# Performance work log

Measured on AMD Instinct MI355X. Metric: run time of the kernel, lower is better.

Reference implementation:

```python
import jax, jax.numpy as jnp
import numpy as np

NUM_SENSORS = 4
D_MODEL = 64
N_HEAD = 8
HEAD_DIM = 8
EPS_LN = 1e-5
EPS_BN = 1e-5
A_BASE = np.array([[1, 1, 0, 0], [1, 1, 1, 1], [0, 1, 1, 1], [0, 1, 1, 1]], dtype=np.float32)


def _pos_encoding(S, D):
    pos = jnp.arange(S, dtype=jnp.float32)[:, None]
    div = jnp.exp(jnp.arange(0, D, 2, dtype=jnp.float32) * (-jnp.log(jnp.float32(10000.0)) / D))
    pe = jnp.zeros((S, D), jnp.float32)
    pe = pe.at[:, 0::2].set(jnp.sin(pos * div))
    pe = pe.at[:, 1::2].set(jnp.cos(pos * div))
    return pe


def _ln(x, g, b):
    m = x.mean(-1, keepdims=True)
    v = ((x - m) ** 2).mean(-1, keepdims=True)
    return (x - m) * jax.lax.rsqrt(v + EPS_LN) * g + b


def _conv1d(x, w, b, stride, pad):
    y = jax.lax.conv_general_dilated(x, w, (stride,), [(pad, pad)], dimension_numbers=('NCH', 'OIH', 'NCH'))
    return y + b[None, :, None]


def _maxpool2(x):  # [B,C,L] -> [B,C,L//2]
    B, C, L = x.shape
    return x[:, :, : (L // 2) * 2].reshape(B, C, L // 2, 2).max(-1)


def _bn_eval(x, g, b):  # eval-mode BN with fresh running stats (mean=0, var=1)
    scale = g * jax.lax.rsqrt(jnp.float32(1.0 + EPS_BN))
    return x * scale[None, :, None] + b[None, :, None]


def _mha(x, wqkv, bqkv, wo, bo):
    B, S, D = x.shape
    qkv = x @ wqkv.T + bqkv  # [B,S,3D]
    q, k, v = jnp.split(qkv, 3, -1)
    heads = lambda t: t.reshape(B, S, N_HEAD, HEAD_DIM).transpose(0, 2, 1, 3)
    q, k, v = heads(q), heads(k), heads(v)
    scores = jnp.einsum('bhqd,bhkd->bhqk', q, k) / jnp.float32(np.sqrt(HEAD_DIM))
    attn = jax.nn.softmax(scores, -1)
    out = jnp.einsum('bhqk,bhkd->bhqd', attn, v).transpose(0, 2, 1, 3).reshape(B, S, D)
    return out @ wo.T + bo


def _encoder_layer(x, wqkv, bqkv, wo, bo, ln1g, ln1b, w1, b1, w2, b2, ln2g, ln2b):
    # torch post-norm (norm_first=False), gelu, dropout off (eval)
    x = _ln(x + _mha(x, wqkv, bqkv, wo, bo), ln1g, ln1b)
    ff = jax.nn.gelu(x @ w1.T + b1, approximate=False) @ w2.T + b2
    return _ln(x + ff, ln2g, ln2b)


def _branch(x, bp):
    h = x.transpose(0, 2, 1)  # [B,1,L]
    h = _maxpool2(jax.nn.relu(_bn_eval(_conv1d(h, bp['c1w'], bp['c1b'], 2, 2), bp['g1'], bp['be1'])))
    h = _maxpool2(jax.nn.relu(_bn_eval(_conv1d(h, bp['c2w'], bp['c2b'], 1, 1), bp['g2'], bp['be2'])))
    h = h.transpose(0, 2, 1)  # [B,S,64], S = L/8
    h = h + _pos_encoding(h.shape[1], D_MODEL)
    for l in range(2):
        h = _encoder_layer(h, bp['wqkv'][l], bp['bqkv'][l], bp['wo'][l], bp['bo'][l],
                           bp['ln1g'][l], bp['ln1b'][l], bp['fw1'][l], bp['fb1'][l],
                           bp['fw2'][l], bp['fb2'][l], bp['ln2g'][l], bp['ln2b'][l])
    return h.mean(1)  # [B,64]


def _gcn(x, A, W, b):
    # PyG GCNConv with edge weights over the dense per-sample 4x4 graph
    deg = A.sum(1)  # deg[b,j] = sum_i A[b,i,j]  (scatter over dst)
    dinv = jnp.where(deg > 0, 1.0 / jnp.sqrt(jnp.where(deg > 0, deg, 1.0)), 0.0)
    norm = dinv[:, :, None] * A * dinv[:, None, :]  # [B,N,N]
    return jnp.einsum('bij,bif->bjf', norm, x @ W) + b


def _forward(sensor_data, conv1_w, conv1_b, bn1_g, bn1_b, conv2_w, conv2_b, bn2_g, bn2_b,
             attn_wqkv, attn_bqkv, attn_wo, attn_bo, ln1_g, ln1_b, ff_w1, ff_b1, ff_w2, ff_b2,
             ln2_g, ln2_b, ws_w, ws_b, b_s, lambda_init, mc_w1, mc_b1, mc_w2, mc_b2,
             gcn1_w, gcn1_b, gcn2_w, gcn2_b, cls_w1, cls_b1, cls_w2, cls_b2, epoch):
    feats = []
    for i in range(NUM_SENSORS):
        bp = dict(c1w=conv1_w[i], c1b=conv1_b[i], g1=bn1_g[i], be1=bn1_b[i],
                  c2w=conv2_w[i], c2b=conv2_b[i], g2=bn2_g[i], be2=bn2_b[i],
                  wqkv=attn_wqkv[i], bqkv=attn_bqkv[i], wo=attn_wo[i], bo=attn_bo[i],
                  ln1g=ln1_g[i], ln1b=ln1_b[i], fw1=ff_w1[i], fb1=ff_b1[i],
                  fw2=ff_w2[i], fb2=ff_b2[i], ln2g=ln2_g[i], ln2b=ln2_b[i])
        feats.append(_branch(sensor_data[i], bp))
    nf = jnp.stack(feats, 1)  # [B,4,64]
    # dynamic adjacency: sigmoid(W_s([f_i;f_j]) + b_s) for all pairs, vectorized
    wa, wb = ws_w[:D_MODEL], ws_w[D_MODEL:]
    fa = nf @ wa  # [B,4]
    fb = nf @ wb
    s = jax.nn.sigmoid(fa[:, :, None] + fb[:, None, :] + ws_b + b_s)  # [B,4,4]
    deg = s.sum(-1)  # row degree deg[b,i]
    a = s / (deg[:, None, :] + 1e-8)  # == bmm(s, eye * 1/(deg+eps))
    S_hat = jax.nn.relu(a * jnp.asarray(A_BASE))
    lam = jax.nn.sigmoid(jax.nn.relu(nf.mean(1) @ mc_w1.T + mc_b1) @ mc_w2 + mc_b2) * lambda_init  # [B]
    lam = lam[:, None, None]
    A = lam * jnp.eye(NUM_SENSORS, dtype=jnp.float32) + (1.0 - lam) * S_hat  # A_prev = I (first call)
    # tau_0 is undefined in the source; tau treated as 0 => threshold is a no-op (A >= 0)
    h = jax.nn.relu(_gcn(nf, A, gcn1_w, gcn1_b))  # [B,4,128]
    g = _gcn(h, A, gcn2_w, gcn2_b).mean(1)  # [B,256]
    return jax.nn.relu(g @ cls_w1 + cls_b1) @ cls_w2 + cls_b2  # [B,5]


def setup_inputs() -> dict:
    key = jax.random.key(0)
    ks = iter(jax.random.split(key, 64))
    rn = lambda shape, s: jax.random.normal(next(ks), shape, jnp.float32) * s
    S4, B, L = 4, 64, 2048
    return {
        'sensor_data': jax.random.normal(next(ks), (S4, B, L, 1), jnp.float32),
        'conv1_w': rn((S4, 32, 1, 5), 0.3), 'conv1_b': rn((S4, 32), 0.02),
        'bn1_g': jnp.ones((S4, 32), jnp.float32), 'bn1_b': jnp.zeros((S4, 32), jnp.float32),
        'conv2_w': rn((S4, 64, 32, 3), 0.1), 'conv2_b': rn((S4, 64), 0.02),
        'bn2_g': jnp.ones((S4, 64), jnp.float32), 'bn2_b': jnp.zeros((S4, 64), jnp.float32),
        'attn_wqkv': rn((S4, 2, 192, 64), 0.08), 'attn_bqkv': rn((S4, 2, 192), 0.02),
        'attn_wo': rn((S4, 2, 64, 64), 0.08), 'attn_bo': rn((S4, 2, 64), 0.02),
        'ln1_g': jnp.ones((S4, 2, 64), jnp.float32), 'ln1_b': jnp.zeros((S4, 2, 64), jnp.float32),
        'ff_w1': rn((S4, 2, 256, 64), 0.08), 'ff_b1': rn((S4, 2, 256), 0.02),
        'ff_w2': rn((S4, 2, 64, 256), 0.06), 'ff_b2': rn((S4, 2, 64), 0.02),
        'ln2_g': jnp.ones((S4, 2, 64), jnp.float32), 'ln2_b': jnp.zeros((S4, 2, 64), jnp.float32),
        'ws_w': rn((128,), 0.08), 'ws_b': rn((), 0.02), 'b_s': jnp.zeros((), jnp.float32),
        'lambda_init': jnp.asarray(0.5, jnp.float32),
        'mc_w1': rn((32, 64), 0.1), 'mc_b1': rn((32,), 0.02),
        'mc_w2': rn((32,), 0.15), 'mc_b2': rn((), 0.02),
        'gcn1_w': rn((64, 128), 0.1), 'gcn1_b': rn((128,), 0.02),
        'gcn2_w': rn((128, 256), 0.08), 'gcn2_b': rn((256,), 0.02),
        'cls_w1': rn((256, 128), 0.08), 'cls_b1': rn((128,), 0.02),
        'cls_w2': rn((128, 5), 0.1), 'cls_b2': rn((5,), 0.02),
        'epoch': 1,
    }


def reference(sensor_data, conv1_w, conv1_b, bn1_g, bn1_b, conv2_w, conv2_b, bn2_g, bn2_b,
              attn_wqkv, attn_bqkv, attn_wo, attn_bo, ln1_g, ln1_b, ff_w1, ff_b1, ff_w2, ff_b2,
              ln2_g, ln2_b, ws_w, ws_b, b_s, lambda_init, mc_w1, mc_b1, mc_w2, mc_b2,
              gcn1_w, gcn1_b, gcn2_w, gcn2_b, cls_w1, cls_b1, cls_w2, cls_b2, epoch):
    return _forward(sensor_data, conv1_w, conv1_b, bn1_g, bn1_b, conv2_w, conv2_b, bn2_g, bn2_b,
                    attn_wqkv, attn_bqkv, attn_wo, attn_bo, ln1_g, ln1_b, ff_w1, ff_b1, ff_w2, ff_b2,
                    ln2_g, ln2_b, ws_w, ws_b, b_s, lambda_init, mc_w1, mc_b1, mc_w2, mc_b2,
                    gcn1_w, gcn1_b, gcn2_w, gcn2_b, cls_w1, cls_b1, cls_w2, cls_b2, epoch)
```

## Files before the change

kernel.cpp:

```cpp
#include <hip/hip_runtime.h>
#include <hip/hip_fp16.h>

#define NSENS 4
#define NB    64
#define LIN   2048
#define C1N   32
#define LP1   512
#define C2N   64
#define SEQ   256
#define DM    64

typedef _Float16 f16x4 __attribute__((ext_vector_type(4)));
typedef _Float16 f16x8 __attribute__((ext_vector_type(8)));
typedef float    f32x4 __attribute__((ext_vector_type(4)));

#define MFMA16(A,B,C) __builtin_amdgcn_mfma_f32_16x16x16f16((A),(B),(C),0,0,0)
#define MFMA32(A,B,C) __builtin_amdgcn_mfma_f32_16x16x32_f16((A),(B),(C),0,0,0)

__device__ __forceinline__ float fast_exp2(float x) {
#if __has_builtin(__builtin_amdgcn_exp2f)
  return __builtin_amdgcn_exp2f(x);
#else
  return exp2f(x);
#endif
}

__device__ __forceinline__ char* swp(char* base, int row, int stride, int byteoff) {
  return base + row*stride + ((byteoff & ~15) ^ ((row & 7) << 4)) + (byteoff & 15);
}
__device__ __forceinline__ float sr_h(char* base, int row, int stride, int col) {
  return (float)*(const _Float16*)swp(base, row, stride, col*2);
}
__device__ __forceinline__ void pack8(char* p, float4 a, float4 b) {
  __half2 h0 = __floats2half2_rn(a.x,a.y), h1 = __floats2half2_rn(a.z,a.w);
  __half2 h2 = __floats2half2_rn(b.x,b.y), h3 = __floats2half2_rn(b.z,b.w);
  uint4 u; u.x=*(unsigned*)&h0; u.y=*(unsigned*)&h1; u.z=*(unsigned*)&h2; u.w=*(unsigned*)&h3;
  *(uint4*)p = u;
}
__device__ __forceinline__ uint2 pack4u(float a, float b, float cc, float d) {
  __half2 h0 = __floats2half2_rn(a, b), h1 = __floats2half2_rn(cc, d);
  uint2 u; u.x = *(unsigned*)&h0; u.y = *(unsigned*)&h1; return u;
}

__global__ __launch_bounds__(256) void wprep_kernel(
    const float* __restrict__ wqkv, const float* __restrict__ wo,
    const float* __restrict__ fw1,  const float* __restrict__ fw2,
    unsigned short* __restrict__ w16)
{
  const int wi = blockIdx.x;
  unsigned short* dst = w16 + (size_t)wi*49152;
  const float* s0 = wqkv + (size_t)wi*12288;
  const float* s1 = wo   + (size_t)wi*4096;
  const float* s2 = fw1  + (size_t)wi*16384;
  const float* s3 = fw2  + (size_t)wi*16384;
  for (int i = threadIdx.x; i < 12288; i += 256) { __half h = __float2half_rn(s0[i]); dst[i]       = *(unsigned short*)&h; }
  for (int i = threadIdx.x; i < 4096;  i += 256) { __half h = __float2half_rn(s1[i]); dst[12288+i] = *(unsigned short*)&h; }
  for (int i = threadIdx.x; i < 16384; i += 256) { __half h = __float2half_rn(s2[i]); dst[16384+i] = *(unsigned short*)&h; }
  for (int i = threadIdx.x; i < 16384; i += 256) { __half h = __float2half_rn(s3[i]); dst[32768+i] = *(unsigned short*)&h; }
}

__global__ __launch_bounds__(1024, 1) void tx_kernel(
  const float* __restrict__ sens,
  const float* __restrict__ c1w, const float* __restrict__ c1b,
  const float* __restrict__ bn1g, const float* __restrict__ bn1b,
  const float* __restrict__ c2w, const float* __restrict__ c2b,
  const float* __restrict__ bn2g, const float* __restrict__ bn2b,
  float* __restrict__ nf,
  const unsigned short* __restrict__ w16,
  const float* __restrict__ bqkv, const float* __restrict__ bo,
  const float* __restrict__ ln1g, const float* __restrict__ ln1b,
  const float* __restrict__ fb1,  const float* __restrict__ fb2,
  const float* __restrict__ ln2g, const float* __restrict__ ln2b)
{
  __shared__ char smem[132096];
  char* xs = smem;
  char* Qb = smem + 32768;
  char* Kb = smem + 65536;
  char* Vt = smem + 98304;
  float* red = (float*)(smem + 131072);

  const int bid = blockIdx.x;
  const int s = bid >> 6, b = bid & 63;
  const int t = threadIdx.x;
  const int l = t & 63, w = t >> 6;
  const int g = l >> 4, c = l & 15;
  const int m0 = w * 16;
  const float qs = 0.35355339059327373f * 1.4426950408889634f;

  {
    __half (*h1p)[516] = (__half(*)[516])(smem + 32768);
    float* w2s = (float*)(smem + 65792);

    for (int i = t; i < C1N*3*C2N; i += 1024) {
      int co = i & 63; int rem = i >> 6; int k = rem % 3; int ci = rem / 3;
      w2s[(ci*3 + k)*64 + co] = c2w[((s*C2N + co)*C1N + ci)*3 + k];
    }
    const float* xg = sens + (size_t)(s*NB + b)*LIN;
    const float bnr = rsqrtf(1.0f + 1e-5f);
    {
      const int cc1 = t & 31;
      const int l0 = t >> 5;
      const float w0 = c1w[(s*C1N + cc1)*5 + 0];
      const float w1 = c1w[(s*C1N + cc1)*5 + 1];
      const float w2 = c1w[(s*C1N + cc1)*5 + 2];
      const float w3 = c1w[(s*C1N + cc1)*5 + 3];
      const float w4 = c1w[(s*C1N + cc1)*5 + 4];
      const float cb = c1b[s*C1N + cc1];
      const float sc = bn1g[s*C1N + cc1]*bnr;
      const float bt = bn1b[s*C1N + cc1];
      for (int ll = l0; ll < LP1; ll += 32) {
        const int base = 4*ll;
        float xm2 = (base-2 >= 0) ? xg[base-2] : 0.f;
        float xm1 = (base-1 >= 0) ? xg[base-1] : 0.f;
        float x0v = xg[base+0];
        float x1v = xg[base+1];
        float x2v = xg[base+2];
        float x3v = xg[base+3];
        float x4v = (base+4 < LIN) ? xg[base+4] : 0.f;
        float y0 = w0*xm2 + w1*xm1 + w2*x0v + w3*x1v + w4*x2v;
        float y1 = w0*x0v + w1*x1v + w2*x2v + w3*x3v + w4*x4v;
        y0 = (y0 + cb)*sc + bt;
        y1 = (y1 + cb)*sc + bt;
        h1p[cc1][ll+1] = __float2half(fmaxf(fmaxf(y0, y1), 0.f));
        if (ll == 0)      h1p[cc1][0]      = __float2half(0.f);
        if (ll == LP1-1)  h1p[cc1][LP1+1]  = __float2half(0.f);
      }
    }
    __syncthreads();
    {
      const int r = t & 255, q = t >> 8;
      float acc0[16], acc1[16];
      #pragma unroll
      for (int i = 0; i < 16; ++i) { acc0[i] = 0.f; acc1[i] = 0.f; }
      for (int ci = 0; ci < C1N; ++ci) {
        const __half2 a01 = *(const __half2*)&h1p[ci][2*r];
        const __half2 a23 = *(const __half2*)&h1p[ci][2*r+2];
        const float2 f01 = __half22float2(a01);
        const float2 f23 = __half22float2(a23);
        const float hx[4] = { f01.x, f01.y, f23.x, f23.y };
        #pragma unroll
        for (int k = 0; k < 3; ++k) {
          const float* wrow = w2s + (ci*3+k)*64 + q*16;
          const float4 wv0 = *(const float4*)(wrow + 0);
          const float4 wv1 = *(const float4*)(wrow + 4);
          const float4 wv2 = *(const float4*)(wrow + 8);
          const float4 wv3 = *(const float4*)(wrow + 12);
          const float wr[16] = {wv0.x,wv0.y,wv0.z,wv0.w, wv1.x,wv1.y,wv1.z,wv1.w,
                                wv2.x,wv2.y,wv2.z,wv2.w, wv3.x,wv3.y,wv3.z,wv3.w};
          const float xa = hx[k], xb = hx[k+1];
          #pragma unroll
          for (int i = 0; i < 16; ++i) {
            acc0[i] = fmaf(wr[i], xa, acc0[i]);
            acc1[i] = fmaf(wr[i], xb, acc1[i]);
          }
        }
      }
      float vv[16];
      #pragma unroll
      for (int i = 0; i < 16; ++i) {
        const int d = q*16 + i;
        const float cb2 = c2b[s*C2N + d];
        const float sc2 = bn2g[s*C2N + d]*bnr;
        const float bt2 = bn2b[s*C2N + d];
        float v0 = (acc0[i] + cb2)*sc2 + bt2;
        float v1 = (acc1[i] + cb2)*sc2 + bt2;
        float v = fmaxf(fmaxf(v0, v1), 0.f);
        const float ang = (float)r * __expf(-0.14391156463f*(float)(d & ~1));
        const float pe = (d & 1) ? cosf(ang) : sinf(ang);
        vv[i] = v + pe;
      }
      pack8(swp(xs, r, 128, q*32),
            make_float4(vv[0],vv[1],vv[2],vv[3]), make_float4(vv[4],vv[5],vv[6],vv[7]));
      pack8(swp(xs, r, 128, q*32 + 16),
            make_float4(vv[8],vv[9],vv[10],vv[11]), make_float4(vv[12],vv[13],vv[14],vv[15]));
    }
  }
  __syncthreads();

  for (int layer = 0; layer < 2; ++layer) {
    const int wi = s*2 + layer;
    const unsigned short* wq = w16 + (size_t)wi*49152;
    const unsigned short* wo = wq + 12288;
    const unsigned short* w1 = wq + 16384;
    const unsigned short* w2 = wq + 32768;
    const float* Bq  = bqkv + wi*192;
    const float* Bo  = bo   + wi*64;
    const float* G1  = ln1g + wi*64; const float* B1 = ln1b + wi*64;
    const float* Bf1 = fb1  + wi*256; const float* Bf2 = fb2 + wi*64;
    const float* G2  = ln2g + wi*64; const float* B2 = ln2b + wi*64;

    {
      f16x8 xf0 = *(const f16x8*)swp(xs, m0+c, 128, 0  + g*16);
      f16x8 xf1 = *(const f16x8*)swp(xs, m0+c, 128, 64 + g*16);
      #pragma unroll
      for (int nt = 0; nt < 4; ++nt) {
        const int row = 64 + nt*16 + c;
        f16x8 w0f = *(const f16x8*)(wq + row*64 + 8*g);
        f16x8 w1f = *(const f16x8*)(wq + row*64 + 32 + 8*g);
        f32x4 d = {0.f,0.f,0.f,0.f};
        d = MFMA32(w0f, xf0, d); d = MFMA32(w1f, xf1, d);
        float4 b4 = *(const float4*)(Bq + 64 + nt*16 + 4*g);
        *(uint2*)swp(Kb, m0+c, 128, nt*32 + 8*g) =
            pack4u(d[0]+b4.x, d[1]+b4.y, d[2]+b4.z, d[3]+b4.w);
      }
      #pragma unroll
      for (int nt = 0; nt < 4; ++nt) {
        const int row = nt*16 + c;
        f16x8 w0f = *(const f16x8*)(wq + row*64 + 8*g);
        f16x8 w1f = *(const f16x8*)(wq + row*64 + 32 + 8*g);
        f32x4 d = {0.f,0.f,0.f,0.f};
        d = MFMA32(w0f, xf0, d); d = MFMA32(w1f, xf1, d);
        float4 b4 = *(const float4*)(Bq + nt*16 + 4*g);
        *(uint2*)swp(Qb, m0+c, 128, nt*32 + 8*g) =
            pack4u((d[0]+b4.x)*qs, (d[1]+b4.y)*qs, (d[2]+b4.z)*qs, (d[3]+b4.w)*qs);
      }
      #pragma unroll
      for (int nt = 0; nt < 4; ++nt) {
        const int row = 128 + nt*16 + c;
        f16x8 w0f = *(const f16x8*)(wq + row*64 + 8*g);
        f16x8 w1f = *(const f16x8*)(wq + row*64 + 32 + 8*g);
        f32x4 d = {0.f,0.f,0.f,0.f};
        d = MFMA32(xf0, w0f, d); d = MFMA32(xf1, w1f, d);
        const float bias = Bq[128 + nt*16 + c];
        *(uint2*)swp(Vt, nt*16+c, 512, 32*w + 8*g) =
            pack4u(d[0]+bias, d[1]+bias, d[2]+bias, d[3]+bias);
      }
    }
    __syncthreads();

    #pragma unroll 2
    for (int task = 0; task < 8; ++task) {
      const int h = task;
      f16x4 qb = {0,0,0,0};
      if (g < 2) qb = *(const f16x4*)swp(Qb, m0+c, 128, 16*h + 8*g);
      f32x4 o = {0.f,0.f,0.f,0.f};
      #pragma unroll
      for (int jt = 0; jt < 16; ++jt) {
        f16x4 ka = *(const f16x4*)swp(Kb, jt*16+c, 128, (16*h + 8*g) & 127);
        f32x4 st = {0.f,0.f,0.f,0.f};
        st = MFMA16(ka, qb, st);
        uint2 pu = pack4u(fast_exp2(st[0]), fast_exp2(st[1]),
                          fast_exp2(st[2]), fast_exp2(st[3]));
        f16x4 pb = *(f16x4*)&pu;
        f16x4 va;
        if (c < 8) va = *(const f16x4*)swp(Vt, 8*h+c, 512, jt*32 + (g>>1)*16 + (g&1)*8);
        else { va[0]=(_Float16)1.f; va[1]=(_Float16)1.f; va[2]=(_Float16)1.f; va[3]=(_Float16)1.f; }
        o = MFMA16(va, pb, o);
      }
      const float den = __shfl(o[0], 32 + c, 64);
      const float rinv = 1.0f / den;
      if (g < 2) {
        *(uint2*)swp(Qb, m0+c, 128, 16*h + 8*g) =
            pack4u(o[0]*rinv, o[1]*rinv, o[2]*rinv, o[3]*rinv);
      }
    }
    __syncthreads();

    {
      f16x8 ab0 = *(const f16x8*)swp(Qb, m0+c, 128, 0  + g*16);
      f16x8 ab1 = *(const f16x8*)swp(Qb, m0+c, 128, 64 + g*16);
      float vals[4][4];
      #pragma unroll
      for (int nt = 0; nt < 4; ++nt) {
        f16x8 w0f = *(const f16x8*)(wo + (nt*16+c)*64 + 8*g);
        f16x8 w1f = *(const f16x8*)(wo + (nt*16+c)*64 + 32 + 8*g);
        f32x4 d = {0.f,0.f,0.f,0.f};
        d = MFMA32(w0f, ab0, d); d = MFMA32(w1f, ab1, d);
        float4 b4 = *(const float4*)(Bo + nt*16 + 4*g);
        uint2 rr = *(uint2*)swp(xs, m0+c, 128, nt*32 + 8*g);
        float2 r0 = __half22float2(*(__half2*)&rr.x);
        float2 r1 = __half22float2(*(__half2*)&rr.y);
        vals[nt][0] = d[0] + b4.x + r0.x;
        vals[nt][1] = d[1] + b4.y + r0.y;
        vals[nt][2] = d[2] + b4.z + r1.x;
        vals[nt][3] = d[3] + b4.w + r1.y;
      }
      float p1 = 0.f, p2 = 0.f;
      #pragma unroll
      for (int nt = 0; nt < 4; ++nt)
        #pragma unroll
        for (int i = 0; i < 4; ++i) { p1 += vals[nt][i]; p2 = fmaf(vals[nt][i], vals[nt][i], p2); }
      p1 += __shfl_xor(p1, 16, 64); p1 += __shfl_xor(p1, 32, 64);
      p2 += __shfl_xor(p2, 16, 64); p2 += __shfl_xor(p2, 32, 64);
      const float mean = p1*(1.0f/64.0f);
      const float rstd = rsqrtf(p2*(1.0f/64.0f) - mean*mean + 1e-5f);
      #pragma unroll
      for (int nt = 0; nt < 4; ++nt) {
        float4 g4 = *(const float4*)(G1 + nt*16 + 4*g);
        float4 b4 = *(const float4*)(B1 + nt*16 + 4*g);
        *(uint2*)swp(xs, m0+c, 128, nt*32 + 8*g) =
            pack4u((vals[nt][0]-mean)*rstd*g4.x + b4.x,
                   (vals[nt][1]-mean)*rstd*g4.y + b4.y,
                   (vals[nt][2]-mean)*rstd*g4.z + b4.z,
                   (vals[nt][3]-mean)*rstd*g4.w + b4.w);
      }
    }

    {
      f16x8 xb0 = *(const f16x8*)swp(xs, m0+c, 128, 0  + g*16);
      f16x8 xb1 = *(const f16x8*)swp(xs, m0+c, 128, 64 + g*16);
      f32x4 o2[4];
      #pragma unroll
      for (int nt2 = 0; nt2 < 4; ++nt2) { o2[nt2][0]=0.f; o2[nt2][1]=0.f; o2[nt2][2]=0.f; o2[nt2][3]=0.f; }
      #pragma unroll
      for (int ht = 0; ht < 16; ++ht) {
        f16x8 w0f = *(const f16x8*)(w1 + (ht*16+c)*64 + 8*g);
        f16x8 w1f = *(const f16x8*)(w1 + (ht*16+c)*64 + 32 + 8*g);
        f32x4 d = {0.f,0.f,0.f,0.f};
        d = MFMA32(w0f, xb0, d); d = MFMA32(w1f, xb1, d);
        float4 bf4 = *(const float4*)(Bf1 + ht*16 + 4*g);
        float h0 = d[0] + bf4.x, h1 = d[1] + bf4.y, h2 = d[2] + bf4.z, h3 = d[3] + bf4.w;
        h0 = 0.5f*h0*(1.0f + erff(h0*0.70710678118654752f));
        h1 = 0.5f*h1*(1.0f + erff(h1*0.70710678118654752f));
        h2 = 0.5f*h2*(1.0f + erff(h2*0.70710678118654752f));
        h3 = 0.5f*h3*(1.0f + erff(h3*0.70710678118654752f));
        uint2 pu = pack4u(h0, h1, h2, h3);
        f16x4 pf = *(f16x4*)&pu;
        #pragma unroll
        for (int nt2 = 0; nt2 < 4; ++nt2) {
          f16x4 a2 = *(const f16x4*)(w2 + (nt2*16+c)*256 + ht*16 + 4*g);
          o2[nt2] = MFMA16(a2, pf, o2[nt2]);
        }
      }
      float vals[4][4];
      #pragma unroll
      for (int nt2 = 0; nt2 < 4; ++nt2) {
        float4 b4 = *(const float4*)(Bf2 + nt2*16 + 4*g);
        uint2 rr = *(uint2*)swp(xs, m0+c, 128, nt2*32 + 8*g);
        float2 r0 = __half22float2(*(__half2*)&rr.x);
        float2 r1 = __half22float2(*(__half2*)&rr.y);
        vals[nt2][0] = o2[nt2][0] + b4.x + r0.x;
        vals[nt2][1] = o2[nt2][1] + b4.y + r0.y;
        vals[nt2][2] = o2[nt2][2] + b4.z + r1.x;
        vals[nt2][3] = o2[nt2][3] + b4.w + r1.y;
      }
      float p1 = 0.f, p2 = 0.f;
      #pragma unroll
      for (int nt2 = 0; nt2 < 4; ++nt2)
        #pragma unroll
        for (int i = 0; i < 4; ++i) { p1 += vals[nt2][i]; p2 = fmaf(vals[nt2][i], vals[nt2][i], p2); }
      p1 += __shfl_xor(p1, 16, 64); p1 += __shfl_xor(p1, 32, 64);
      p2 += __shfl_xor(p2, 16, 64); p2 += __shfl_xor(p2, 32, 64);
      const float mean = p1*(1.0f/64.0f);
      const float rstd = rsqrtf(p2*(1.0f/64.0f) - mean*mean + 1e-5f);
      #pragma unroll
      for (int nt2 = 0; nt2 < 4; ++nt2) {
        float4 g4 = *(const float4*)(G2 + nt2*16 + 4*g);
        float4 b4 = *(const float4*)(B2 + nt2*16 + 4*g);
        *(uint2*)swp(xs, m0+c, 128, nt2*32 + 8*g) =
            pack4u((vals[nt2][0]-mean)*rstd*g4.x + b4.x,
                   (vals[nt2][1]-mean)*rstd*g4.y + b4.y,
                   (vals[nt2][2]-mean)*rstd*g4.z + b4.z,
                   (vals[nt2][3]-mean)*rstd*g4.w + b4.w);
      }
    }
  }

  __syncthreads();
  if (t < 256) {
    const int d = t & 63, qu = t >> 6;
    float sm = 0.f;
    for (int rr = qu*64; rr < qu*64 + 64; ++rr) sm += sr_h(xs, rr, 128, d);
    red[qu*64 + d] = sm;
  }
  __syncthreads();
  if (t < 64) {
    float sm = red[t] + red[64+t] + red[128+t] + red[192+t];
    nf[((size_t)b*4 + s)*64 + t] = sm * (1.0f/256.0f);
  }
}

__global__ __launch_bounds__(128) void head_kernel(
  const float* __restrict__ nf,
  const float* __restrict__ ws_w, const float* __restrict__ ws_b,
  const float* __restrict__ b_s,  const float* __restrict__ lambda_init,
  const float* __restrict__ mc_w1, const float* __restrict__ mc_b1,
  const float* __restrict__ mc_w2, const float* __restrict__ mc_b2,
  const float* __restrict__ g1w, const float* __restrict__ g1b,
  const float* __restrict__ g2w, const float* __restrict__ g2b,
  const float* __restrict__ cw1, const float* __restrict__ cb1,
  const float* __restrict__ cw2, const float* __restrict__ cb2,
  float* __restrict__ out)
{
  const int b = blockIdx.x, t = threadIdx.x;
  __shared__ float nfb[256];
  __shared__ float meannf[64];
  __shared__ float fafb[8];
  __shared__ float z1[32];
  __shared__ float normM[16];
  __shared__ float rs[4];
  __shared__ float xw[512];
  __shared__ float hmat[512];
  __shared__ float hw[1024];
  __shared__ float gv[256];
  __shared__ float r1[128];

  for (int i = t; i < 256; i += 128) nfb[i] = nf[b*256 + i];
  __syncthreads();
  if (t < 8) {
    const int i = t & 3;
    const float* w = ws_w + (t >> 2)*64;
    float acc = 0.f;
    for (int c = 0; c < 64; ++c) acc = fmaf(nfb[i*64+c], w[c], acc);
    fafb[t] = acc;
  }
  if (t >= 64 && t < 128) {
    const int d = t - 64;
    meannf[d] = 0.25f*(nfb[d] + nfb[64+d] + nfb[128+d] + nfb[192+d]);
  }
  __syncthreads();
  if (t < 32) {
    float acc = mc_b1[t];
    const float* w = mc_w1 + t*64;
    for (int c = 0; c < 64; ++c) acc = fmaf(meannf[c], w[c], acc);
    z1[t] = fmaxf(acc, 0.f);
  }
  __syncthreads();
  if (t == 0) {
    float li = mc_b2[0];
    for (int k = 0; k < 32; ++k) li = fmaf(z1[k], mc_w2[k], li);
    const float lam = (1.0f/(1.0f + __expf(-li))) * lambda_init[0];
    const float AB[4][4] = {{1,1,0,0},{1,1,1,1},{0,1,1,1},{0,1,1,1}};
    const float add = ws_b[0] + b_s[0];
    float sM[4][4], deg[4];
    for (int i = 0; i < 4; ++i) {
      float d_ = 0.f;
      for (int j = 0; j < 4; ++j) {
        sM[i][j] = 1.0f/(1.0f + __expf(-(fafb[i] + fafb[4+j] + add)));
        d_ += sM[i][j];
      }
      deg[i] = d_;
    }
    float A[4][4], dinv[4];
    for (int i = 0; i < 4; ++i)
      for (int j = 0; j < 4; ++j) {
        const float a_ = sM[i][j] / (deg[j] + 1e-8f);
        const float sh = fmaxf(a_ * AB[i][j], 0.f);
        A[i][j] = lam*((i==j) ? 1.f : 0.f) + (1.0f - lam)*sh;
      }
    for (int j = 0; j < 4; ++j) {
      float d_ = 0.f;
      for (int i = 0; i < 4; ++i) d_ += A[i][j];
      dinv[j] = (d_ > 0.f) ? rsqrtf(d_) : 0.f;
    }
    for (int i = 0; i < 4; ++i) {
      float r_ = 0.f;
      for (int j = 0; j < 4; ++j) {
        const float n_ = dinv[i]*A[i][j]*dinv[j];
        normM[i*4+j] = n_;
        r_ += n_;
      }
      rs[i] = r_;
    }
  }
  __syncthreads();
  for (int idx = t; idx < 512; idx += 128) {
    const int i = idx >> 7, f = idx & 127;
    float acc = 0.f;
    for (int c = 0; c < 64; ++c) acc = fmaf(nfb[i*64+c], g1w[c*128 + f], acc);
    xw[idx] = acc;
  }
  __syncthreads();
  for (int idx = t; idx < 512; idx += 128) {
    const int j = idx >> 7, f = idx & 127;
    float acc = g1b[f];
    #pragma unroll
    for (int i = 0; i < 4; ++i) acc = fmaf(normM[i*4+j], xw[i*128+f], acc);
    hmat[j*128+f] = fmaxf(acc, 0.f);
  }
  __syncthreads();
  for (int idx = t; idx < 1024; idx += 128) {
    const int i = idx >> 8, f = idx & 255;
    float acc = 0.f;
    for (int c = 0; c < 128; ++c) acc = fmaf(hmat[i*128+c], g2w[c*256+f], acc);
    hw[idx] = acc;
  }
  __syncthreads();
  for (int f = t; f < 256; f += 128) {
    float acc = 0.f;
    #pragma unroll
    for (int i = 0; i < 4; ++i) acc = fmaf(rs[i], hw[i*256+f], acc);
    gv[f] = 0.25f*acc + g2b[f];
  }
  __syncthreads();
  if (t < 128) {
    float acc = cb1[t];
    for (int c = 0; c < 256; ++c) acc = fmaf(gv[c], cw1[c*128+t], acc);
    r1[t] = fmaxf(acc, 0.f);
  }
  __syncthreads();
  if (t < 5) {
    float acc = cb2[t];
    for (int k = 0; k < 128; ++k) acc = fmaf(r1[k], cw2[k*5 + t], acc);
    out[b*5 + t] = acc;
  }
}

extern "C" void kernel_launch(void* const* d_in, const int* in_sizes, int n_in,
                              void* d_out, int out_size, void* d_ws, size_t ws_size,
                              hipStream_t stream) {
  (void)in_sizes; (void)n_in; (void)out_size; (void)ws_size;
  const float* sens   = (const float*)d_in[0];
  const float* c1w    = (const float*)d_in[1];
  const float* c1b    = (const float*)d_in[2];
  const float* bn1g   = (const float*)d_in[3];
  const float* bn1b   = (const float*)d_in[4];
  const float* c2w    = (const float*)d_in[5];
  const float* c2b    = (const float*)d_in[6];
  const float* bn2g   = (const float*)d_in[7];
  const float* bn2b   = (const float*)d_in[8];
  const float* wqkv   = (const float*)d_in[9];
  const float* bqkv   = (const float*)d_in[10];
  const float* wo     = (const float*)d_in[11];
  const float* bo     = (const float*)d_in[12];
  const float* ln1g   = (const float*)d_in[13];
  const float* ln1b   = (const float*)d_in[14];
  const float* fw1    = (const float*)d_in[15];
  const float* fb1    = (const float*)d_in[16];
  const float* fw2    = (const float*)d_in[17];
  const float* fb2    = (const float*)d_in[18];
  const float* ln2g   = (const float*)d_in[19];
  const float* ln2b   = (const float*)d_in[20];
  const float* ws_w   = (const float*)d_in[21];
  const float* ws_b   = (const float*)d_in[22];
  const float* b_s    = (const float*)d_in[23];
  const float* lam0   = (const float*)d_in[24];
  const float* mc_w1  = (const float*)d_in[25];
  const float* mc_b1  = (const float*)d_in[26];
  const float* mc_w2  = (const float*)d_in[27];
  const float* mc_b2  = (const float*)d_in[28];
  const float* g1w    = (const float*)d_in[29];
  const float* g1b    = (const float*)d_in[30];
  const float* g2w    = (const float*)d_in[31];
  const float* g2b    = (const float*)d_in[32];
  const float* cw1    = (const float*)d_in[33];
  const float* cb1    = (const float*)d_in[34];
  const float* cw2    = (const float*)d_in[35];
  const float* cb2    = (const float*)d_in[36];

  float*          nf  = (float*)d_ws;
  unsigned short* w16 = (unsigned short*)((char*)d_ws + 65536);

  wprep_kernel<<<8, 256, 0, stream>>>(wqkv, wo, fw1, fw2, w16);
  tx_kernel<<<NSENS*NB, 1024, 0, stream>>>(sens, c1w, c1b, bn1g, bn1b,
                                           c2w, c2b, bn2g, bn2b,
                                           nf, w16, bqkv, bo,
                                           ln1g, ln1b, fb1, fb2, ln2g, ln2b);
  head_kernel<<<NB, 128, 0, stream>>>(nf, ws_w, ws_b, b_s, lam0,
                                      mc_w1, mc_b1, mc_w2, mc_b2,
                                      g1w, g1b, g2w, g2b, cw1, cb1, cw2, cb2,
                                      (float*)d_out);
}
```

Measured before the change: 265.3 us.

## Compute conv2 stage with MFMA and split attention PV accumulator chain

Replaces the scalar FP32 FMA loop for the second conv layer with fp16 MFMA 16x16x32 instructions. The conv1 output is stored position-major with channels contiguous, and conv2 weights are transposed to fp16 in shared memory so each of the three kernel taps becomes a small GEMM. The epilogue (bias, BN, ReLU, maxpool, positional encoding) is reworked to match the MFMA output layout and writes individual fp16 elements. The attention PV loop also alternates between two accumulators to break the serial MFMA dependency chain. This adds fp16 rounding of the conv2 weights and scattered 2-byte LDS stores.

```diff
diff --git a/kernel.cpp b/kernel.cpp
--- a/kernel.cpp
+++ b/kernel.cpp
@@ -30,12 +30,6 @@
 }
 __device__ __forceinline__ float sr_h(char* base, int row, int stride, int col) {
   return (float)*(const _Float16*)swp(base, row, stride, col*2);
-}
-__device__ __forceinline__ void pack8(char* p, float4 a, float4 b) {
-  __half2 h0 = __floats2half2_rn(a.x,a.y), h1 = __floats2half2_rn(a.z,a.w);
-  __half2 h2 = __floats2half2_rn(b.x,b.y), h3 = __floats2half2_rn(b.z,b.w);
-  uint4 u; u.x=*(unsigned*)&h0; u.y=*(unsigned*)&h1; u.z=*(unsigned*)&h2; u.w=*(unsigned*)&h3;
-  *(uint4*)p = u;
 }
 __device__ __forceinline__ uint2 pack4u(float a, float b, float cc, float d) {
   __half2 h0 = __floats2half2_rn(a, b), h1 = __floats2half2_rn(cc, d);
@@ -88,26 +82,28 @@
   const float qs = 0.35355339059327373f * 1.4426950408889634f;
 
   {
-    __half (*h1p)[516] = (__half(*)[516])(smem + 32768);
-    float* w2s = (float*)(smem + 65792);
-
-    for (int i = t; i < C1N*3*C2N; i += 1024) {
-      int co = i & 63; int rem = i >> 6; int k = rem % 3; int ci = rem / 3;
-      w2s[(ci*3 + k)*64 + co] = c2w[((s*C2N + co)*C1N + ci)*3 + k];
-    }
+    __half* h1t  = (__half*)(smem + 32768);
+    __half* w2hT = (__half*)(smem + 65664);
+
+    for (int i = t; i < 3*64*32; i += 1024) {
+      const int ci = i & 31; const int rem = i >> 5; const int co = rem & 63; const int k = rem >> 6;
+      w2hT[i] = __float2half_rn(c2w[((s*C2N + co)*C1N + ci)*3 + k]);
+    }
+    if (t < 32) { h1t[t] = __float2half(0.f); h1t[513*32 + t] = __float2half(0.f); }
+
     const float* xg = sens + (size_t)(s*NB + b)*LIN;
     const float bnr = rsqrtf(1.0f + 1e-5f);
     {
-      const int cc1 = t & 31;
+      const int ch = t & 31;
       const int l0 = t >> 5;
-      const float w0 = c1w[(s*C1N + cc1)*5 + 0];
-      const float w1 = c1w[(s*C1N + cc1)*5 + 1];
-      const float w2 = c1w[(s*C1N + cc1)*5 + 2];
-      const float w3 = c1w[(s*C1N + cc1)*5 + 3];
-      const float w4 = c1w[(s*C1N + cc1)*5 + 4];
-      const float cb = c1b[s*C1N + cc1];
-      const float sc = bn1g[s*C1N + cc1]*bnr;
-      const float bt = bn1b[s*C1N + cc1];
+      const float w0 = c1w[(s*C1N + ch)*5 + 0];
+      const float w1 = c1w[(s*C1N + ch)*5 + 1];
+      const float w2 = c1w[(s*C1N + ch)*5 + 2];
+      const float w3 = c1w[(s*C1N + ch)*5 + 3];
+      const float w4 = c1w[(s*C1N + ch)*5 + 4];
+      const float cb = c1b[s*C1N + ch];
+      const float sc = bn1g[s*C1N + ch]*bnr;
+      const float bt = bn1b[s*C1N + ch];
       for (int ll = l0; ll < LP1; ll += 32) {
         const int base = 4*ll;
         float xm2 = (base-2 >= 0) ? xg[base-2] : 0.f;
@@ -121,58 +117,45 @@
         float y1 = w0*x0v + w1*x1v + w2*x2v + w3*x3v + w4*x4v;
         y0 = (y0 + cb)*sc + bt;
         y1 = (y1 + cb)*sc + bt;
-        h1p[cc1][ll+1] = __float2half(fmaxf(fmaxf(y0, y1), 0.f));
-        if (ll == 0)      h1p[cc1][0]      = __float2half(0.f);
-        if (ll == LP1-1)  h1p[cc1][LP1+1]  = __float2half(0.f);
+        h1t[(ll+1)*32 + ch] = __float2half(fmaxf(fmaxf(y0, y1), 0.f));
       }
     }
     __syncthreads();
     {
-      const int r = t & 255, q = t >> 8;
-      float acc0[16], acc1[16];
-      #pragma unroll
-      for (int i = 0; i < 16; ++i) { acc0[i] = 0.f; acc1[i] = 0.f; }
-      for (int ci = 0; ci < C1N; ++ci) {
-        const __half2 a01 = *(const __half2*)&h1p[ci][2*r];
-        const __half2 a23 = *(const __half2*)&h1p[ci][2*r+2];
-        const float2 f01 = __half22float2(a01);
-        const float2 f23 = __half22float2(a23);
-        const float hx[4] = { f01.x, f01.y, f23.x, f23.y };
+      const int p0a = m0*2, p0b = m0*2 + 16;
+      f16x8 aA[3], aB[3];
+      #pragma unroll
+      for (int k = 0; k < 3; ++k) {
+        aA[k] = *(const f16x8*)&h1t[(p0a + c + k)*32 + 8*g];
+        aB[k] = *(const f16x8*)&h1t[(p0b + c + k)*32 + 8*g];
+      }
+      #pragma unroll
+      for (int ct = 0; ct < 4; ++ct) {
+        f32x4 dA = {0.f,0.f,0.f,0.f}, dB = {0.f,0.f,0.f,0.f};
         #pragma unroll
         for (int k = 0; k < 3; ++k) {
-          const float* wrow = w2s + (ci*3+k)*64 + q*16;
-          const float4 wv0 = *(const float4*)(wrow + 0);
-          const float4 wv1 = *(const float4*)(wrow + 4);
-          const float4 wv2 = *(const float4*)(wrow + 8);
-          const float4 wv3 = *(const float4*)(wrow + 12);
-          const float wr[16] = {wv0.x,wv0.y,wv0.z,wv0.w, wv1.x,wv1.y,wv1.z,wv1.w,
-                                wv2.x,wv2.y,wv2.z,wv2.w, wv3.x,wv3.y,wv3.z,wv3.w};
-          const float xa = hx[k], xb = hx[k+1];
-          #pragma unroll
-          for (int i = 0; i < 16; ++i) {
-            acc0[i] = fmaf(wr[i], xa, acc0[i]);
-            acc1[i] = fmaf(wr[i], xb, acc1[i]);
-          }
+          f16x8 bw = *(const f16x8*)&w2hT[(k*64 + ct*16 + c)*32 + 8*g];
+          dA = MFMA32(aA[k], bw, dA);
+          dB = MFMA32(aB[k], bw, dB);
         }
-      }
-      float vv[16];
-      #pragma unroll
-      for (int i = 0; i < 16; ++i) {
-        const int d = q*16 + i;
+        const int d = ct*16 + c;
         const float cb2 = c2b[s*C2N + d];
         const float sc2 = bn2g[s*C2N + d]*bnr;
         const float bt2 = bn2b[s*C2N + d];
-        float v0 = (acc0[i] + cb2)*sc2 + bt2;
-        float v1 = (acc1[i] + cb2)*sc2 + bt2;
-        float v = fmaxf(fmaxf(v0, v1), 0.f);
-        const float ang = (float)r * __expf(-0.14391156463f*(float)(d & ~1));
-        const float pe = (d & 1) ? cosf(ang) : sinf(ang);
-        vv[i] = v + pe;
-      }
-      pack8(swp(xs, r, 128, q*32),
-            make_float4(vv[0],vv[1],vv[2],vv[3]), make_float4(vv[4],vv[5],vv[6],vv[7]));
-      pack8(swp(xs, r, 128, q*32 + 16),
-            make_float4(vv[8],vv[9],vv[10],vv[11]), make_float4(vv[12],vv[13],vv[14],vv[15]));
+        const float efac = __expf(-0.14391156463f*(float)(d & ~1));
+        float v[4];
+        v[0] = fmaxf(fmaxf((dA[0]+cb2)*sc2+bt2, (dA[1]+cb2)*sc2+bt2), 0.f);
+        v[1] = fmaxf(fmaxf((dA[2]+cb2)*sc2+bt2, (dA[3]+cb2)*sc2+bt2), 0.f);
+        v[2] = fmaxf(fmaxf((dB[0]+cb2)*sc2+bt2, (dB[1]+cb2)*sc2+bt2), 0.f);
+        v[3] = fmaxf(fmaxf((dB[2]+cb2)*sc2+bt2, (dB[3]+cb2)*sc2+bt2), 0.f);
+        const int rr[4] = { m0+2*g, m0+2*g+1, m0+8+2*g, m0+8+2*g+1 };
+        #pragma unroll
+        for (int i = 0; i < 4; ++i) {
+          const float ang = (float)rr[i] * efac;
+          const float pe = (d & 1) ? cosf(ang) : sinf(ang);
+          *(_Float16*)swp(xs, rr[i], 128, d*2) = (_Float16)(v[i] + pe);
+        }
+      }
     }
   }
   __syncthreads();
@@ -233,7 +216,7 @@
       const int h = task;
       f16x4 qb = {0,0,0,0};
       if (g < 2) qb = *(const f16x4*)swp(Qb, m0+c, 128, 16*h + 8*g);
-      f32x4 o = {0.f,0.f,0.f,0.f};
+      f32x4 oA = {0.f,0.f,0.f,0.f}, oB = {0.f,0.f,0.f,0.f};
       #pragma unroll
       for (int jt = 0; jt < 16; ++jt) {
         f16x4 ka = *(const f16x4*)swp(Kb, jt*16+c, 128, (16*h + 8*g) & 127);
@@ -245,8 +228,11 @@
         f16x4 va;
         if (c < 8) va = *(const f16x4*)swp(Vt, 8*h+c, 512, jt*32 + (g>>1)*16 + (g&1)*8);
         else { va[0]=(_Float16)1.f; va[1]=(_Float16)1.f; va[2]=(_Float16)1.f; va[3]=(_Float16)1.f; }
-        o = MFMA16(va, pb, o);
-      }
+        if (jt & 1) oB = MFMA16(va, pb, oB);
+        else        oA = MFMA16(va, pb, oA);
+      }
+      f32x4 o;
+      o[0] = oA[0]+oB[0]; o[1] = oA[1]+oB[1]; o[2] = oA[2]+oB[2]; o[3] = oA[3]+oB[3];
       const float den = __shfl(o[0], 32 + c, 64);
       const float rinv = 1.0f / den;
       if (g < 2) {
```

Result: faster. 230.7 us (-13.1%).
